# Kernel optimization log

Measured on AMD Instinct MI355X. Metric: run time of the kernel, lower is better.

Reference implementation:

```python
import jax, jax.numpy as jnp
import numpy as np

BS, TS, NE, ED = 32, 64, 64, 96
E = 256        # attn_embed_dim
H = 4          # attn_n_heads
HD = E // H    # head dim
RNN_H = 256
N_ACT = 32
NA = 16        # n_agents


def setup_inputs():
    key = jax.random.key(0)
    ks = jax.random.split(key, 40)
    entities = jax.random.normal(ks[0], (BS, TS, NE, ED), jnp.float32)
    obs_mask = jax.random.randint(ks[1], (BS, TS, NE, NE), 0, 2).astype(jnp.float32)  # 1 = masked
    entity_mask = (jax.random.uniform(ks[2], (BS, TS, NE)) < 0.1).astype(jnp.float32)  # 1 = inactive
    hidden_state = jnp.zeros((BS * NA, RNN_H), jnp.float32)
    it = iter(range(3, 40))
    def lin(fi, fo):
        return jax.random.normal(ks[next(it)], (fi, fo), jnp.float32) / np.sqrt(fi).astype(np.float32)
    p = dict(
        fc1_w=lin(ED, E), fc1_b=jnp.zeros((E,), jnp.float32),
        attn_in_w=lin(E, 3 * E), attn_out_w=lin(E, E), attn_out_b=jnp.zeros((E,), jnp.float32),
        fc2_w=lin(2 * E, RNN_H), fc2_b=jnp.zeros((RNN_H,), jnp.float32),
        gru_w_ih=lin(RNN_H, 3 * RNN_H), gru_w_hh=lin(RNN_H, 3 * RNN_H),
        gru_b_ih=jnp.zeros((3 * RNN_H,), jnp.float32), gru_b_hh=jnp.zeros((3 * RNN_H,), jnp.float32),
        fc3_w=lin(RNN_H, N_ACT), fc3_b=jnp.zeros((N_ACT,), jnp.float32),
        fcmsg1_w=lin(ED, E), fcmsg1_b=jnp.zeros((E,), jnp.float32),
        lmsg_in_w=lin(E, 3 * E), lmsg_out_w=lin(E, E), lmsg_out_b=jnp.zeros((E,), jnp.float32),
        gmsg_in_w=lin(E, 3 * E), gmsg_out_w=lin(E, E), gmsg_out_b=jnp.zeros((E,), jnp.float32),
        gate_in_w=lin(E, 3 * E), gate_out_w=lin(E, E), gate_out_b=jnp.zeros((E,), jnp.float32),
        gatefc1_w=lin(ED, E), gatefc1_b=jnp.zeros((E,), jnp.float32),
        gatefc2_w=lin(E, 2), gatefc2_b=jnp.zeros((2,), jnp.float32),
    )
    return dict(entities=entities, obs_mask=obs_mask, entity_mask=entity_mask,
                hidden_state=hidden_state, **p)


def _attn(x, in_w, out_w, out_b, pre_mask, post_mask):
    """REFIL EntityAttentionLayer: n_queries = NA agent rows, masks use 1 = masked."""
    B, ne, e = x.shape
    q, k, v = jnp.split(x @ in_w, 3, axis=-1)                       # each [B, ne, E]
    q = q[:, :NA].reshape(B, NA, H, HD).transpose(0, 2, 1, 3)        # [B, H, NA, HD]
    k = k.reshape(B, ne, H, HD).transpose(0, 2, 1, 3)                # [B, H, ne, HD]
    v = v.reshape(B, ne, H, HD).transpose(0, 2, 1, 3)
    logits = jnp.einsum('bhqd,bhkd->bhqk', q, k) / jnp.asarray(np.sqrt(HD), x.dtype)
    m = pre_mask[:, None, :NA, :]                                    # [B, 1, NA, ne]
    logits = jnp.where(m > 0, jnp.asarray(-1e9, x.dtype), logits)
    # softmax; zeroing masked cols also reproduces torch's NaN->0 for fully-masked rows
    w = jax.nn.softmax(logits, axis=-1) * (1.0 - m)
    out = jnp.einsum('bhqk,bhkd->bhqd', w, v).transpose(0, 2, 1, 3).reshape(B, NA, e)
    out = out @ out_w + out_b
    return out * (1.0 - post_mask[..., None])                        # masked_fill(post_mask, 0)


def _forward(entities, obs_mask, entity_mask, hidden_state,
             fc1_w, fc1_b, attn_in_w, attn_out_w, attn_out_b, fc2_w, fc2_b,
             gru_w_ih, gru_w_hh, gru_b_ih, gru_b_hh, fc3_w, fc3_b,
             fcmsg1_w, fcmsg1_b, lmsg_in_w, lmsg_out_w, lmsg_out_b,
             gmsg_in_w, gmsg_out_w, gmsg_out_b, gate_in_w, gate_out_w, gate_out_b,
             gatefc1_w, gatefc1_b, gatefc2_w, gatefc2_b):
    bs, ts, ne, ed = entities.shape
    B = bs * ts
    ent = entities.reshape(B, ne, ed)
    om = obs_mask.reshape(B, ne, ne)
    em = entity_mask.reshape(B, ne)
    agent_mask = em[:, :NA]                                          # [B, NA]
    full_obs_mask = 1.0 - (1.0 - agent_mask[:, None, :]) * (1.0 - agent_mask[:, :, None])

    x1 = jax.nn.relu(ent @ fc1_w + fc1_b)
    x2 = _attn(x1, attn_in_w, attn_out_w, attn_out_b, om, agent_mask)          # [B, NA, E]

    x1_msg = jax.nn.relu(ent @ fcmsg1_w + fcmsg1_b)
    x1_gate = jax.nn.relu(ent @ gatefc1_w + gatefc1_b)
    x2_msg = _attn(x1_msg, lmsg_in_w, lmsg_out_w, lmsg_out_b, om, agent_mask)  # [B, NA, E]
    x2_gate = _attn(x1_gate, gate_in_w, gate_out_w, gate_out_b, om, agent_mask)
    x2_gate = x2_gate @ gatefc2_w + gatefc2_b                                   # [B, NA, 2]

    # argmax of softmax == argmax of logits; gate in {0,1}, non-differentiable
    gate = jnp.argmax(x2_gate, axis=-1).astype(entities.dtype)
    gated_msg = x2_msg * gate[..., None]
    global_msg = _attn(gated_msg, gmsg_in_w, gmsg_out_w, gmsg_out_b,
                       full_obs_mask, agent_mask)                               # [B, NA, E]

    x3 = jax.nn.relu(jnp.concatenate([x2, global_msg], axis=-1) @ fc2_w + fc2_b)
    x3 = x3.reshape(bs, ts, NA, RNN_H)

    # GRU recurrence over ts via scan; hidden flattened to [bs*NA, RNN_H]
    h0 = hidden_state.reshape(-1, RNN_H)
    xs = x3.transpose(1, 0, 2, 3).reshape(ts, bs * NA, RNN_H)

    def step(h, x):
        gi = x @ gru_w_ih + gru_b_ih
        gh = h @ gru_w_hh + gru_b_hh
        ir, iz, inn = jnp.split(gi, 3, axis=-1)
        hr, hz, hn = jnp.split(gh, 3, axis=-1)
        r = jax.nn.sigmoid(ir + hr)
        z = jax.nn.sigmoid(iz + hz)
        n = jnp.tanh(inn + r * hn)
        h_new = (1.0 - z) * n + z * h
        return h_new, h_new

    _, hs = jax.lax.scan(step, h0, xs)                               # [ts, bs*NA, RNN_H]
    hs = hs.reshape(ts, bs, NA, RNN_H).transpose(1, 0, 2, 3)         # [bs, ts, NA, RNN_H]

    q = hs @ fc3_w + fc3_b                                           # [bs, ts, NA, N_ACT]
    am = agent_mask.reshape(bs, ts, NA, 1)
    q = q * (1.0 - am)                                               # masked_fill(agent_mask, 0)
    return q, hs, x2_gate


def reference(entities, obs_mask, entity_mask, hidden_state,
              fc1_w, fc1_b, attn_in_w, attn_out_w, attn_out_b, fc2_w, fc2_b,
              gru_w_ih, gru_w_hh, gru_b_ih, gru_b_hh, fc3_w, fc3_b,
              fcmsg1_w, fcmsg1_b, lmsg_in_w, lmsg_out_w, lmsg_out_b,
              gmsg_in_w, gmsg_out_w, gmsg_out_b, gate_in_w, gate_out_w, gate_out_b,
              gatefc1_w, gatefc1_b, gatefc2_w, gatefc2_b):
    return _forward(entities, obs_mask, entity_mask, hidden_state,
                    fc1_w, fc1_b, attn_in_w, attn_out_w, attn_out_b, fc2_w, fc2_b,
                    gru_w_ih, gru_w_hh, gru_b_ih, gru_b_hh, fc3_w, fc3_b,
                    fcmsg1_w, fcmsg1_b, lmsg_in_w, lmsg_out_w, lmsg_out_b,
                    gmsg_in_w, gmsg_out_w, gmsg_out_b, gate_in_w, gate_out_w, gate_out_b,
                    gatefc1_w, gatefc1_b, gatefc2_w, gatefc2_b)
```

## Files before the change

### kernel.cpp

```cpp
#include <hip/hip_runtime.h>


#define DEV __device__ __forceinline__

typedef _Float16 f16x8 __attribute__((ext_vector_type(8)));
typedef _Float16 f16x4 __attribute__((ext_vector_type(4)));
typedef float    f32x4 __attribute__((ext_vector_type(4)));
typedef float    f32x16 __attribute__((ext_vector_type(16)));

DEV f32x4 mfma16(f16x8 a, f16x8 b, f32x4 c){
  return __builtin_amdgcn_mfma_f32_16x16x32_f16(a, b, c, 0, 0, 0);
}
DEV f32x16 mfma32(f16x8 a, f16x8 b, f32x16 c){
  return __builtin_amdgcn_mfma_f32_32x32x16_f16(a, b, c, 0, 0, 0);
}

template<int MODE> struct AB {
  f16x8 hi, lo;
  DEV void mf(const AB& b, f32x4& c) const {
    if constexpr (MODE){
      c = mfma16(lo, b.hi, c);
      c = mfma16(hi, b.lo, c);
    }
    c = mfma16(hi, b.hi, c);
  }
};

template<int MODE> DEV AB<MODE> ldW(const _Float16* p, int losz){
  AB<MODE> r; r.hi = *(const f16x8*)p;
  if constexpr (MODE) r.lo = *(const f16x8*)(p + losz);
  return r;
}
template<int MODE> DEV AB<MODE> ldL(const _Float16* ph, const _Float16* pl){
  AB<MODE> r; r.hi = *(const f16x8*)ph;
  if constexpr (MODE) r.lo = *(const f16x8*)pl;
  return r;
}
template<int MODE> DEV AB<MODE> ldF(const float* p){
  AB<MODE> r;
  f32x4 v0 = *(const f32x4*)p, v1 = *(const f32x4*)(p + 4);
#pragma unroll
  for (int i = 0; i < 4; ++i){
    float a = v0[i], b = v1[i];
    _Float16 ah = (_Float16)a, bh = (_Float16)b;
    r.hi[i] = ah; r.hi[i+4] = bh;
    if constexpr (MODE){
      r.lo[i]   = (_Float16)(a - (float)ah);
      r.lo[i+4] = (_Float16)(b - (float)bh);
    }
  }
  return r;
}
template<int MODE> DEV void stL(_Float16* ph, _Float16* pl, int idx, float v){
  _Float16 h = (_Float16)v;
  ph[idx] = h;
  if constexpr (MODE) pl[idx] = (_Float16)(v - (float)h);
}

struct WJobs {
  const float* src[15];
  unsigned off[15];
  int K[15], N[15], mode[15];
};

__global__ __launch_bounds__(256) void k0_conv(WJobs jb, char* ws){
  const int job = blockIdx.y;
  const int K = jb.K[job], N = jb.N[job];
  const int total = K * N;
  _Float16* dh = (_Float16*)(ws + jb.off[job]);
  const float* src = jb.src[job];
  const int m = jb.mode[job];
  for (int idx = blockIdx.x*256 + threadIdx.x; idx < total; idx += gridDim.x*256){
    int n = idx / K, k = idx - n*K;
    float v = src[(size_t)k*N + n];
    _Float16 h = (_Float16)v;
    dh[idx] = h;
    if (m) dh[total + idx] = (_Float16)(v - (float)h);
  }
}

__global__ __launch_bounds__(256) void k0w_gate(
    const float* __restrict__ Wout, const float* __restrict__ Wg2,
    const float* __restrict__ bo,   const float* __restrict__ Win,
    _Float16* __restrict__ wveff, float* __restrict__ beff)
{
  __shared__ float weff_s[256*2];
  const int tid = threadIdx.x;
  {
    float a0 = 0.f, a1 = 0.f;
    const float* wr = Wout + (size_t)tid*256;
    for (int f = 0; f < 256; ++f){ float x = wr[f]; a0 += x*Wg2[2*f]; a1 += x*Wg2[2*f+1]; }
    weff_s[tid*2] = a0; weff_s[tid*2+1] = a1;
  }
  if (tid < 2){
    float s = 0.f;
    for (int f = 0; f < 256; ++f) s += bo[f]*Wg2[2*f + tid];
    beff[tid] = s;
  }
  __syncthreads();
  {
    const int j = tid;
    for (int n = 0; n < 16; ++n){
      float v = 0.f;
      if (n < 8){
        int h = n >> 1, c = n & 1;
        const float* wr = Win + (size_t)j*768 + 512 + h*64;
        const float* we = weff_s + (h*64)*2 + c;
        for (int d = 0; d < 64; ++d) v += wr[d]*we[2*d];
      }
      _Float16 hi = (_Float16)v;
      wveff[n*256 + j] = hi;
      wveff[16*256 + n*256 + j] = (_Float16)(v - (float)hi);
    }
  }
}

__global__ __launch_bounds__(512) void k1_all(
    const float* __restrict__ ent, const float* __restrict__ om, const float* __restrict__ em,
    const _Float16* __restrict__ W1a, const float* __restrict__ b1a,
    const _Float16* __restrict__ WINa,
    const _Float16* __restrict__ WOUTa, const float* __restrict__ boa,
    float* __restrict__ x2outa,
    const _Float16* __restrict__ W1b, const float* __restrict__ b1b,
    const _Float16* __restrict__ WINb,
    const _Float16* __restrict__ WOUTb, const float* __restrict__ bob,
    float* __restrict__ x2outb,
    const _Float16* __restrict__ W1g, const float* __restrict__ b1g,
    const _Float16* __restrict__ WINg,
    const _Float16* __restrict__ WVEFF,
    const float* __restrict__ beff, const float* __restrict__ gb2,
    float* __restrict__ og, float* __restrict__ gate)
{
  const int tid = threadIdx.x;
  const int w = tid >> 6, lg = (tid >> 4) & 3, li = tid & 15;
  extern __shared__ char smem[];

  if (blockIdx.x < 2048){
    const int br = blockIdx.x >> 10;
    const int p  = blockIdx.x & 1023;
    const int bb2[2] = { 2*p, 2*p + 1 };
    const _Float16* W1   = br ? W1b   : W1a;
    const float*    b1   = br ? b1b   : b1a;
    const _Float16* WIN  = br ? WINb  : WINa;
    const _Float16* WOUT = br ? WOUTb : WOUTa;
    const float*    bo   = br ? bob   : boa;
    float*          x2out= br ? x2outb: x2outa;

    const int wi = w & 3, ih = w >> 2;
    const int l = tid & 63;
    const int r32 = l & 31, kh = (l >> 5)*8;

    _Float16* x1   = (_Float16*)smem;
    _Float16* Ks   = (_Float16*)(smem + 67584);
    _Float16* Vs   = (_Float16*)(smem + 86016);
    _Float16* Qful = (_Float16*)(smem + 104448);
    float*    lgs  = (float*)(smem + 121344);
    _Float16* Ps   = (_Float16*)(smem + 130560);
    _Float16* outp = (_Float16*)(smem + 135168);

    {
      const int b = bb2[ih];
      _Float16* x1p = x1 + ih*16896;
      const int mt = wi & 1, ntb = (wi >> 1)*4;
      f32x16 acc0 = 0.f, acc1 = 0.f, acc2 = 0.f, acc3 = 0.f;
#pragma unroll
      for (int kk = 0; kk < 6; ++kk){
        AB<0> a = ldF<0>(ent + ((size_t)b*64 + mt*32 + r32)*96 + kk*16 + kh);
        f16x8 B0 = *(const f16x8*)(W1 + (size_t)((ntb + 0)*32 + r32)*96 + kk*16 + kh);
        f16x8 B1 = *(const f16x8*)(W1 + (size_t)((ntb + 1)*32 + r32)*96 + kk*16 + kh);
        f16x8 B2 = *(const f16x8*)(W1 + (size_t)((ntb + 2)*32 + r32)*96 + kk*16 + kh);
        f16x8 B3 = *(const f16x8*)(W1 + (size_t)((ntb + 3)*32 + r32)*96 + kk*16 + kh);
        acc0 = mfma32(a.hi, B0, acc0);
        acc1 = mfma32(a.hi, B1, acc1);
        acc2 = mfma32(a.hi, B2, acc2);
        acc3 = mfma32(a.hi, B3, acc3);
      }
#pragma unroll
      for (int s = 0; s < 4; ++s){
        const f32x16& ac = (s == 0) ? acc0 : (s == 1) ? acc1 : (s == 2) ? acc2 : acc3;
        int col = (ntb + s)*32 + r32;
        float bias = b1[col];
#pragma unroll
        for (int reg = 0; reg < 16; ++reg){
          int row = (reg & 3) + 8*(reg >> 2) + 4*(l >> 5);
          x1p[(mt*32 + row)*264 + col] = (_Float16)fmaxf(ac[reg] + bias, 0.f);
        }
      }
    }
    __syncthreads();

    {
      f32x16 acc = 0.f;
      const int itq = r32 >> 4, qr = r32 & 15;
      for (int kk = 0; kk < 16; ++kk){
        f16x8 A = *(const f16x8*)(x1 + itq*16896 + qr*264 + kk*16 + kh);
        f16x8 B = *(const f16x8*)(WIN + (size_t)(w*32 + r32)*256 + kk*16 + kh);
        acc = mfma32(A, B, acc);
      }
#pragma unroll
      for (int reg = 0; reg < 16; ++reg){
        int row = (reg & 3) + 8*(reg >> 2) + 4*(l >> 5);
        Qful[(row >> 4)*4224 + (row & 15)*264 + w*32 + r32] = (_Float16)acc[reg];
      }
    }
    __syncthreads();

    for (int h = 0; h < 4; ++h){
      if (w < 4){
        const int kt = w >> 1, dt = w & 1;
        f32x16 acc0 = 0.f, acc1 = 0.f;
        for (int kk = 0; kk < 16; ++kk){
          int ao = (kt*32 + r32)*264 + kk*16 + kh;
          f16x8 A0 = *(const f16x8*)(x1 + ao);
          f16x8 A1 = *(const f16x8*)(x1 + 16896 + ao);
          f16x8 B = *(const f16x8*)(WIN + (size_t)(256 + 64*h + dt*32 + r32)*256 + kk*16 + kh);
          acc0 = mfma32(A0, B, acc0);
          acc1 = mfma32(A1, B, acc1);
        }
#pragma unroll
        for (int reg = 0; reg < 16; ++reg){
          int row = (reg & 3) + 8*(reg >> 2) + 4*(l >> 5);
          Ks[(kt*32 + row)*72 + dt*32 + r32]        = (_Float16)acc0[reg];
          Ks[4608 + (kt*32 + row)*72 + dt*32 + r32] = (_Float16)acc1[reg];
        }
      } else {
        const int wv = w - 4;
        const int kt = wv >> 1, dt = wv & 1;
        f32x16 acc0 = 0.f, acc1 = 0.f;
        for (int kk = 0; kk < 16; ++kk){
          int ao = (kt*32 + r32)*264 + kk*16 + kh;
          f16x8 A0 = *(const f16x8*)(x1 + ao);
          f16x8 A1 = *(const f16x8*)(x1 + 16896 + ao);
          f16x8 B = *(const f16x8*)(WIN + (size_t)(512 + 64*h + dt*32 + r32)*256 + kk*16 + kh);
          acc0 = mfma32(A0, B, acc0);
          acc1 = mfma32(A1, B, acc1);
        }
#pragma unroll
        for (int rr = 0; rr < 4; ++rr){
          f16x4 p0, p1;
#pragma unroll
          for (int q4 = 0; q4 < 4; ++q4){
            p0[q4] = (_Float16)acc0[rr*4 + q4];
            p1[q4] = (_Float16)acc1[rr*4 + q4];
          }
          int key = kt*32 + rr*8 + 4*(l >> 5);
          *(f16x4*)(Vs + (dt*32 + r32)*72 + key)        = p0;
          *(f16x4*)(Vs + 4608 + (dt*32 + r32)*72 + key) = p1;
        }
      }
      __syncthreads();
      {
        const int b = bb2[ih];
        f32x4 acc = 0.f;
#pragma unroll
        for (int kk = 0; kk < 2; ++kk){
          f16x8 A = *(const f16x8*)(Qful + ih*4224 + li*264 + 64*h + kk*32 + lg*8);
          f16x8 B = *(const f16x8*)(Ks + ih*4608 + (16*wi + li)*72 + kk*32 + lg*8);
          acc = mfma16(A, B, acc);
        }
#pragma unroll
        for (int j = 0; j < 4; ++j){
          int q = 4*lg + j, key = 16*wi + li;
          float v = acc[j] * 0.125f;
          float m = om[((size_t)b*64 + q)*64 + key];
          if (m > 0.f) v = -1e9f;
          lgs[ih*1152 + q*72 + key] = v;
        }
      }
      __syncthreads();
      {
        const int it = tid >> 8, q = (tid >> 4) & 15, i16 = tid & 15;
        const int b = bb2[it];
        float pv[4], mx = -3e38f;
#pragma unroll
        for (int u = 0; u < 4; ++u){ pv[u] = lgs[it*1152 + q*72 + i16 + 16*u]; mx = fmaxf(mx, pv[u]); }
#pragma unroll
        for (int d = 1; d < 16; d <<= 1) mx = fmaxf(mx, __shfl_xor(mx, d, 16));
        float s = 0.f;
#pragma unroll
        for (int u = 0; u < 4; ++u){ pv[u] = expf(pv[u] - mx); s += pv[u]; }
#pragma unroll
        for (int d = 1; d < 16; d <<= 1) s += __shfl_xor(s, d, 16);
#pragma unroll
        for (int u = 0; u < 4; ++u){
          int key = i16 + 16*u;
          float m = om[((size_t)b*64 + q)*64 + key];
          Ps[it*1152 + q*72 + key] = (_Float16)((pv[u]/s)*(1.f - m));
        }
      }
      __syncthreads();
      {
        f32x4 acc = 0.f;
#pragma unroll
        for (int kk = 0; kk < 2; ++kk){
          f16x8 A = *(const f16x8*)(Ps + ih*1152 + li*72 + kk*32 + lg*8);
          f16x8 B = *(const f16x8*)(Vs + ih*4608 + (16*wi + li)*72 + kk*32 + lg*8);
          acc = mfma16(A, B, acc);
        }
#pragma unroll
        for (int j = 0; j < 4; ++j)
          outp[ih*4224 + (4*lg + j)*264 + 64*h + 16*wi + li] = (_Float16)acc[j];
      }
      __syncthreads();
    }

    {
      f32x16 acc = 0.f;
      const int ito = r32 >> 4, qr = r32 & 15;
      for (int kk = 0; kk < 16; ++kk){
        f16x8 A = *(const f16x8*)(outp + ito*4224 + qr*264 + kk*16 + kh);
        f16x8 B = *(const f16x8*)(WOUT + (size_t)(w*32 + r32)*256 + kk*16 + kh);
        acc = mfma32(A, B, acc);
      }
      int col = w*32 + r32;
      float bias = bo[col];
#pragma unroll
      for (int reg = 0; reg < 16; ++reg){
        int row = (reg & 3) + 8*(reg >> 2) + 4*(l >> 5);
        int it2 = row >> 4, q2 = row & 15;
        const int b = bb2[it2];
        float v = (acc[reg] + bias) * (1.f - em[(size_t)b*64 + q2]);
        x2out[((size_t)b*16 + q2)*256 + col] = v;
      }
    }
    return;
  }

  {
    constexpr int W1SZ = 96*256, WINSZ = 256*768, WVSZ = 16*256;
    const int b = blockIdx.x - 2048;
    const int l = tid & 63;
    const int r32 = l & 31, kh = (l >> 5)*8;

    char* sp = smem;
    _Float16* x1h = (_Float16*)sp; sp += 64*264*2;
    _Float16* x1l = (_Float16*)sp; sp += 64*264*2;
    _Float16* Kh  = (_Float16*)sp; sp += 64*72*2;
    _Float16* Kl  = (_Float16*)sp; sp += 64*72*2;
    _Float16* Qh  = (_Float16*)sp; sp += 16*264*2;
    _Float16* Ql  = (_Float16*)sp; sp += 16*264*2;
    float*    lgs = (float*)sp;    sp += 16*72*4;
    float*    Ps  = (float*)sp;    sp += 16*66*4;
    float*    v2s = (float*)sp;    sp += 64*18*4;
    float*  ogacc = (float*)sp;    sp += 32*4;
    float*  Kpart = (float*)sp;    sp += 8192*4;

    {
      const int mt = w & 1, ntb = (w >> 1)*2;
      f32x16 acc0 = 0.f, acc1 = 0.f;
#pragma unroll
      for (int kk = 0; kk < 6; ++kk){
        AB<1> a = ldF<1>(ent + ((size_t)b*64 + mt*32 + r32)*96 + kk*16 + kh);
#pragma unroll
        for (int s = 0; s < 2; ++s){
          const _Float16* bp = W1g + (size_t)((ntb + s)*32 + r32)*96 + kk*16 + kh;
          f16x8 Bh = *(const f16x8*)bp;
          f16x8 Bl = *(const f16x8*)(bp + W1SZ);
          f32x16& ac = s ? acc1 : acc0;
          ac = mfma32(a.lo, Bh, ac);
          ac = mfma32(a.hi, Bl, ac);
          ac = mfma32(a.hi, Bh, ac);
        }
      }
#pragma unroll
      for (int s = 0; s < 2; ++s){
        const f32x16& ac = s ? acc1 : acc0;
        int col = (ntb + s)*32 + r32;
        float bias = b1g[col];
#pragma unroll
        for (int reg = 0; reg < 16; ++reg){
          int row = (reg & 3) + 8*(reg >> 2) + 4*(l >> 5);
          stL<1>(x1h, x1l, (mt*32 + row)*264 + col, fmaxf(ac[reg] + bias, 0.f));
        }
      }
    }
    if (tid < 32) ogacc[tid] = 0.f;
    __syncthreads();

    {
#pragma unroll
      for (int s = 0; s < 2; ++s){
        int nt = w + s*8;
        f32x4 acc = 0.f;
        for (int kk = 0; kk < 8; ++kk){
          int ao = li*264 + kk*32 + lg*8;
          AB<1> a = ldL<1>(x1h + ao, x1l + ao);
          AB<1> bb = ldW<1>(WINg + (size_t)(nt*16 + li)*256 + kk*32 + lg*8, WINSZ);
          a.mf(bb, acc);
        }
#pragma unroll
        for (int j = 0; j < 4; ++j)
          stL<1>(Qh, Ql, (4*lg + j)*264 + nt*16 + li, acc[j]);
      }
      if (w < 4){
        f32x4 acc = 0.f;
        for (int kk = 0; kk < 8; ++kk){
          int ao = (w*16 + li)*264 + kk*32 + lg*8;
          AB<1> a = ldL<1>(x1h + ao, x1l + ao);
          AB<1> bb = ldW<1>(WVEFF + (size_t)li*256 + kk*32 + lg*8, WVSZ);
          a.mf(bb, acc);
        }
#pragma unroll
        for (int j = 0; j < 4; ++j)
          v2s[(w*16 + 4*lg + j)*18 + li] = acc[j];
      }
    }
    __syncthreads();

    for (int h = 0; h < 4; ++h){
      {
        const int t = w & 3, kt = t >> 1, dt = t & 1, khalf = w >> 2;
        f32x16 acc = 0.f;
#pragma unroll
        for (int k8 = 0; k8 < 8; ++k8){
          int ko = (khalf*8 + k8)*16 + kh;
          int ao = (kt*32 + r32)*264 + ko;
          f16x8 ah = *(const f16x8*)(x1h + ao);
          f16x8 al = *(const f16x8*)(x1l + ao);
          const _Float16* bp = WINg + (size_t)(256 + h*64 + dt*32 + r32)*256 + ko;
          f16x8 Bh = *(const f16x8*)bp;
          f16x8 Bl = *(const f16x8*)(bp + WINSZ);
          acc = mfma32(al, Bh, acc);
          acc = mfma32(ah, Bl, acc);
          acc = mfma32(ah, Bh, acc);
        }
#pragma unroll
        for (int reg = 0; reg < 16; ++reg){
          int row = (reg & 3) + 8*(reg >> 2) + 4*(l >> 5);
          Kpart[((khalf*4 + t)*32 + row)*32 + r32] = acc[reg];
        }
      }
      __syncthreads();
      {
        for (int e = tid; e < 4096; e += 512){
          float s2 = Kpart[e] + Kpart[4096 + e];
          int t2 = e >> 10, idx = e & 1023, row = idx >> 5, col = idx & 31;
          stL<1>(Kh, Kl, ((t2 >> 1)*32 + row)*72 + (t2 & 1)*32 + col, s2);
        }
      }
      __syncthreads();
      if (w < 4){
        f32x4 acc = 0.f;
#pragma unroll
        for (int kk = 0; kk < 2; ++kk){
          int ao = li*264 + h*64 + kk*32 + lg*8;
          AB<1> a = ldL<1>(Qh + ao, Ql + ao);
          int bo_ = (16*w + li)*72 + kk*32 + lg*8;
          AB<1> bb = ldL<1>(Kh + bo_, Kl + bo_);
          a.mf(bb, acc);
        }
#pragma unroll
        for (int j = 0; j < 4; ++j){
          int q = 4*lg + j, key = 16*w + li;
          float v = acc[j] * 0.125f;
          float m = om[((size_t)b*64 + q)*64 + key];
          if (m > 0.f) v = -1e9f;
          lgs[q*72 + key] = v;
        }
      }
      __syncthreads();
      if (tid < 256){
        int q = tid >> 4, i16 = tid & 15;
        float pv[4], mx = -3e38f;
#pragma unroll
        for (int u = 0; u < 4; ++u){ pv[u] = lgs[q*72 + i16 + 16*u]; mx = fmaxf(mx, pv[u]); }
#pragma unroll
        for (int d = 1; d < 16; d <<= 1) mx = fmaxf(mx, __shfl_xor(mx, d, 16));
        float s = 0.f;
#pragma unroll
        for (int u = 0; u < 4; ++u){ pv[u] = expf(pv[u] - mx); s += pv[u]; }
#pragma unroll
        for (int d = 1; d < 16; d <<= 1) s += __shfl_xor(s, d, 16);
#pragma unroll
        for (int u = 0; u < 4; ++u){
          int key = i16 + 16*u;
          float m = om[((size_t)b*64 + q)*64 + key];
          Ps[q*66 + key] = (pv[u]/s)*(1.f - m);
        }
      }
      __syncthreads();
      if (tid < 256){
        int q = tid >> 4, l16 = tid & 15;
        float a0 = 0.f, a1 = 0.f;
#pragma unroll
        for (int u = 0; u < 4; ++u){
          int k = l16 + 16*u;
          float p2 = Ps[q*66 + k];
          a0 += p2 * v2s[k*18 + h*2];
          a1 += p2 * v2s[k*18 + h*2 + 1];
        }
#pragma unroll
        for (int d = 1; d < 16; d <<= 1){ a0 += __shfl_xor(a0, d, 16); a1 += __shfl_xor(a1, d, 16); }
        if (l16 == 0){ ogacc[q*2] += a0; ogacc[q*2 + 1] += a1; }
      }
      __syncthreads();
    }
    if (tid < 16){
      int q = tid;
      float am = em[(size_t)b*64 + q];
      float g0 = (1.f - am)*(ogacc[2*q]     + beff[0]) + gb2[0];
      float g1 = (1.f - am)*(ogacc[2*q + 1] + beff[1]) + gb2[1];
      og[((size_t)b*16 + q)*2]     = g0;
      og[((size_t)b*16 + q)*2 + 1] = g1;
      gate[(size_t)b*16 + q] = (g1 > g0) ? 1.f : 0.f;
    }
  }
}

__global__ __launch_bounds__(256) void k2_global(
    const float* __restrict__ em,
    const float* __restrict__ x2, const float* __restrict__ x2m,
    const float* __restrict__ gate,
    const _Float16* __restrict__ GMIN, const _Float16* __restrict__ GMOUT, const float* __restrict__ gob,
    const _Float16* __restrict__ FC2T, const float* __restrict__ fc2b,
    const _Float16* __restrict__ GIHT, const float* __restrict__ gib,
    float* __restrict__ gi)
{
  const int p = blockIdx.x;
  const int tid = threadIdx.x;
  const int w = tid >> 6, lg = (tid >> 4) & 3, li = tid & 15;
  const int l = tid & 63;
  const int r32 = l & 31, kh = (l >> 5)*8;

  extern __shared__ char smem[];
  float*    gate_s = (float*)smem;
  _Float16* gm_s   = (_Float16*)(smem + 128);
  _Float16* Q2     = (_Float16*)(smem + 17024);
  _Float16* K2s    = (_Float16*)(smem + 21632);
  _Float16* Vt2    = (_Float16*)(smem + 26240);
  float*    lg2    = (float*)(smem + 36480);
  _Float16* P2     = (_Float16*)(smem + 39552);
  _Float16* outp   = (_Float16*)(smem + 42112);
  _Float16* cat_s  = (_Float16*)(smem + 59008);
  _Float16* x3_s   = (_Float16*)(smem + 92288);

  if (tid < 32){
    int it = tid >> 4, q = tid & 15;
    gate_s[it*16 + q] = gate[(size_t)(2*p + it)*16 + q];
  }
  __syncthreads();
#pragma unroll
  for (int it = 0; it < 2; ++it){
    const int b = 2*p + it;
    for (int idx = tid; idx < 4096; idx += 256){
      int q = idx >> 8, d = idx & 255;
      gm_s[it*4224 + q*264 + d]  = (_Float16)(x2m[((size_t)b*16 + q)*256 + d] * gate_s[it*16 + q]);
      cat_s[it*8320 + q*520 + d] = (_Float16)(x2[((size_t)b*16 + q)*256 + d]);
    }
  }
  for (int idx = tid; idx < 2*64*40; idx += 256) Vt2[idx] = (_Float16)0.f;
  for (int idx = tid; idx < 2*16*40; idx += 256) P2[idx] = (_Float16)0.f;
  __syncthreads();
  for (int h = 0; h < 4; ++h){
    {
      f32x4 aq0 = 0.f, aq1 = 0.f, ak0 = 0.f, ak1 = 0.f, av0 = 0.f, av1 = 0.f;
      for (int kk = 0; kk < 8; ++kk){
        f16x8 A0 = *(const f16x8*)(gm_s + li*264 + kk*32 + lg*8);
        f16x8 A1 = *(const f16x8*)(gm_s + 4224 + li*264 + kk*32 + lg*8);
        f16x8 Bq = *(const f16x8*)(GMIN + (size_t)(      64*h + 16*w + li)*256 + kk*32 + lg*8);
        f16x8 Bk = *(const f16x8*)(GMIN + (size_t)(256 + 64*h + 16*w + li)*256 + kk*32 + lg*8);
        f16x8 Bv = *(const f16x8*)(GMIN + (size_t)(512 + 64*h + 16*w + li)*256 + kk*32 + lg*8);
        aq0 = mfma16(A0, Bq, aq0); aq1 = mfma16(A1, Bq, aq1);
        ak0 = mfma16(A0, Bk, ak0); ak1 = mfma16(A1, Bk, ak1);
        av0 = mfma16(A0, Bv, av0); av1 = mfma16(A1, Bv, av1);
      }
#pragma unroll
      for (int j = 0; j < 4; ++j){
        int rw = 4*lg + j, dim = 16*w + li;
        Q2[rw*72 + dim]         = (_Float16)aq0[j];
        Q2[1152 + rw*72 + dim]  = (_Float16)aq1[j];
        K2s[rw*72 + dim]        = (_Float16)ak0[j];
        K2s[1152 + rw*72 + dim] = (_Float16)ak1[j];
        Vt2[dim*40 + rw]        = (_Float16)av0[j];
        Vt2[2560 + dim*40 + rw] = (_Float16)av1[j];
      }
    }
    __syncthreads();
    if (w < 2){
      const int it = w, b = 2*p + it;
      f32x4 acc = 0.f;
#pragma unroll
      for (int kk = 0; kk < 2; ++kk){
        f16x8 A = *(const f16x8*)(Q2  + it*1152 + li*72 + kk*32 + lg*8);
        f16x8 B = *(const f16x8*)(K2s + it*1152 + li*72 + kk*32 + lg*8);
        acc = mfma16(A, B, acc);
      }
      float amk = em[(size_t)b*64 + li];
#pragma unroll
      for (int j = 0; j < 4; ++j){
        int q = 4*lg + j;
        float amq = em[(size_t)b*64 + q];
        float m = 1.f - (1.f - amq)*(1.f - amk);
        float v = acc[j]*0.125f;
        if (m > 0.f) v = -1e9f;
        lg2[it*384 + q*24 + li] = v;
      }
    }
    __syncthreads();
    {
      int q = tid >> 4, key = tid & 15;
#pragma unroll
      for (int it = 0; it < 2; ++it){
        const int b = 2*p + it;
        float v = lg2[it*384 + q*24 + key];
        float mx = v;
#pragma unroll
        for (int d = 1; d < 16; d <<= 1) mx = fmaxf(mx, __shfl_xor(mx, d, 16));
        float pe = expf(v - mx);
        float s = pe;
#pragma unroll
        for (int d = 1; d < 16; d <<= 1) s += __shfl_xor(s, d, 16);
        float amq = em[(size_t)b*64 + q], amk = em[(size_t)b*64 + key];
        float m = 1.f - (1.f - amq)*(1.f - amk);
        P2[it*640 + q*40 + key] = (_Float16)((pe/s)*(1.f - m));
      }
    }
    __syncthreads();
    {
#pragma unroll
      for (int it = 0; it < 2; ++it){
        f32x4 acc = 0.f;
        f16x8 A = *(const f16x8*)(P2 + it*640 + li*40 + lg*8);
        f16x8 B = *(const f16x8*)(Vt2 + it*2560 + (16*w + li)*40 + lg*8);
        acc = mfma16(A, B, acc);
#pragma unroll
        for (int j = 0; j < 4; ++j)
          outp[it*4224 + (4*lg + j)*264 + 64*h + 16*w + li] = (_Float16)acc[j];
      }
    }
    __syncthreads();
  }
  {
    const int ito = r32 >> 4, qr = r32 & 15;
#pragma unroll
    for (int s = 0; s < 2; ++s){
      int nt = 2*w + s;
      f32x16 acc = 0.f;
      for (int kk = 0; kk < 16; ++kk){
        f16x8 A = *(const f16x8*)(outp + ito*4224 + qr*264 + kk*16 + kh);
        f16x8 B = *(const f16x8*)(GMOUT + (size_t)(nt*32 + r32)*256 + kk*16 + kh);
        acc = mfma32(A, B, acc);
      }
      int col = nt*32 + r32;
      float bias = gob[col];
#pragma unroll
      for (int reg = 0; reg < 16; ++reg){
        int row = (reg & 3) + 8*(reg >> 2) + 4*(l >> 5);
        int it2 = row >> 4, q2 = row & 15;
        float m = 1.f - em[(size_t)(2*p + it2)*64 + q2];
        cat_s[it2*8320 + q2*520 + 256 + col] = (_Float16)((acc[reg] + bias)*m);
      }
    }
  }
  __syncthreads();
  {
    const int ito = r32 >> 4, qr = r32 & 15;
#pragma unroll
    for (int s = 0; s < 2; ++s){
      int nt = 2*w + s;
      f32x16 acc = 0.f;
      for (int kk = 0; kk < 32; ++kk){
        f16x8 A = *(const f16x8*)(cat_s + ito*8320 + qr*520 + kk*16 + kh);
        f16x8 B = *(const f16x8*)(FC2T + (size_t)(nt*32 + r32)*512 + kk*16 + kh);
        acc = mfma32(A, B, acc);
      }
      int col = nt*32 + r32;
      float bias = fc2b[col];
#pragma unroll
      for (int reg = 0; reg < 16; ++reg){
        int row = (reg & 3) + 8*(reg >> 2) + 4*(l >> 5);
        int it2 = row >> 4, q2 = row & 15;
        x3_s[it2*4224 + q2*264 + col] = (_Float16)fmaxf(acc[reg] + bias, 0.f);
      }
    }
  }
  __syncthreads();
  {
    const int r0 = ((2*p) >> 6)*16, t0 = (2*p) & 63;
    const int ito = r32 >> 4, qr = r32 & 15;
#pragma unroll
    for (int s = 0; s < 6; ++s){
      int nt = 6*w + s;
      f32x16 acc = 0.f;
      for (int kk = 0; kk < 16; ++kk){
        f16x8 A = *(const f16x8*)(x3_s + ito*4224 + qr*264 + kk*16 + kh);
        f16x8 B = *(const f16x8*)(GIHT + (size_t)(nt*32 + r32)*256 + kk*16 + kh);
        acc = mfma32(A, B, acc);
      }
      int col = nt*32 + r32;
      float bias = gib[col];
#pragma unroll
      for (int reg = 0; reg < 16; ++reg){
        int row = (reg & 3) + 8*(reg >> 2) + 4*(l >> 5);
        int it2 = row >> 4, q2 = row & 15;
        gi[((size_t)((r0 + q2)*64 + t0 + it2))*768 + col] = acc[reg] + bias;
      }
    }
  }
}

__global__ __launch_bounds__(512) void k3_gru(
    const _Float16* __restrict__ WHH, const float* __restrict__ bhh,
    const float* __restrict__ gi, const float* __restrict__ h0,
    float* __restrict__ hs)
{
  const int rb = blockIdx.x;
  const int row0 = rb * 16;
  const int tid = threadIdx.x;
  const int w = tid >> 6, lg = (tid >> 4) & 3, li = tid & 15;

  extern __shared__ char smem3[];
  _Float16* hf16 = (_Float16*)smem3;
  float* hf32 = (float*)(smem3 + 8448);
  float* gh   = (float*)(smem3 + 8448 + 16640);
  float* bhs  = (float*)(smem3 + 8448 + 16640 + 49664);

  for (int idx = tid; idx < 768; idx += 512) bhs[idx] = bhh[idx];
  for (int idx = tid; idx < 4096; idx += 512){
    int r = idx >> 8, d = idx & 255;
    float v = h0[(size_t)(row0 + r)*256 + d];
    hf32[r*260 + d] = v;
    hf16[r*264 + d] = (_Float16)v;
  }
  __syncthreads();

  const int er = tid >> 5;
  const int dd = (tid & 31) * 8;

  for (int t = 0; t < 64; ++t){
    const float* gp = gi + ((size_t)(row0 + er)*64 + t)*768 + dd;
    f32x4 gr[2], gz[2], gn[2];
#pragma unroll
    for (int v = 0; v < 2; ++v){
      gr[v] = *(const f32x4*)(gp + v*4);
      gz[v] = *(const f32x4*)(gp + 256 + v*4);
      gn[v] = *(const f32x4*)(gp + 512 + v*4);
    }
    f16x8 a[8];
#pragma unroll
    for (int kk = 0; kk < 8; ++kk)
      a[kk] = *(const f16x8*)(hf16 + li*264 + kk*32 + lg*8);
    f32x4 acc[6];
#pragma unroll
    for (int c = 0; c < 6; ++c) acc[c] = 0.f;
#pragma unroll
    for (int c = 0; c < 6; ++c){
      const _Float16* bp = WHH + (size_t)(w*96 + c*16 + li)*256 + lg*8;
#pragma unroll
      for (int kk = 0; kk < 8; ++kk)
        acc[c] = mfma16(a[kk], *(const f16x8*)(bp + kk*32), acc[c]);
    }
#pragma unroll
    for (int c = 0; c < 6; ++c){
      int col = w*96 + c*16 + li;
#pragma unroll
      for (int j = 0; j < 4; ++j)
        gh[(4*lg + j)*776 + col] = acc[c][j];
    }
    __syncthreads();
    {
      float* hp32 = hf32 + er*260 + dd;
      float* hsp  = hs + ((size_t)(rb*64 + t)*16 + er)*256 + dd;
      f16x8 hv8;
#pragma unroll
      for (int v = 0; v < 2; ++v){
        f32x4 xr = *(const f32x4*)(gh + er*776 +       dd + v*4);
        f32x4 xz = *(const f32x4*)(gh + er*776 + 256 + dd + v*4);
        f32x4 xn = *(const f32x4*)(gh + er*776 + 512 + dd + v*4);
        f32x4 hold = *(const f32x4*)(hp32 + v*4);
        f32x4 hout;
#pragma unroll
        for (int e = 0; e < 4; ++e){
          int d = dd + v*4 + e;
          float rr_ = 1.f/(1.f + __expf(-(gr[v][e] + xr[e] + bhs[d])));
          float zz  = 1.f/(1.f + __expf(-(gz[v][e] + xz[e] + bhs[256 + d])));
          float pre = gn[v][e] + rr_*(xn[e] + bhs[512 + d]);
          float nn  = 1.f - 2.f/(1.f + __expf(2.f*pre));
          float hv = (1.f - zz)*nn + zz*hold[e];
          hout[e] = hv;
          hv8[v*4 + e] = (_Float16)hv;
        }
        *(f32x4*)(hp32 + v*4) = hout;
        *(f32x4*)(hsp + v*4)  = hout;
      }
      *(f16x8*)(hf16 + er*264 + dd) = hv8;
    }
    __syncthreads();
  }
}

__global__ __launch_bounds__(256) void k4_q(
    const _Float16* __restrict__ FC3T, const float* __restrict__ fc3b,
    const float* __restrict__ em, const float* __restrict__ hs, float* __restrict__ qo)
{
  const int tid = threadIdx.x;
  const int w = tid >> 6, lg = (tid >> 4) & 3, li = tid & 15;
  const int rb = blockIdx.x*64 + 16*w;
  f32x4 acc[2];
#pragma unroll
  for (int c = 0; c < 2; ++c) acc[c] = 0.f;
  for (int kk = 0; kk < 8; ++kk){
    const float* ap = hs + (size_t)(rb + li)*256 + kk*32 + lg*8;
    f32x4 v0 = *(const f32x4*)ap, v1 = *(const f32x4*)(ap + 4);
    f16x8 A;
#pragma unroll
    for (int e = 0; e < 4; ++e){ A[e] = (_Float16)v0[e]; A[e+4] = (_Float16)v1[e]; }
#pragma unroll
    for (int c = 0; c < 2; ++c){
      f16x8 B = *(const f16x8*)(FC3T + (size_t)(16*c + li)*256 + kk*32 + lg*8);
      acc[c] = mfma16(A, B, acc[c]);
    }
  }
#pragma unroll
  for (int c = 0; c < 2; ++c){
    int col = 16*c + li;
    float bias = fc3b[col];
#pragma unroll
    for (int j = 0; j < 4; ++j){
      int row = rb + 4*lg + j;
      float am = em[(size_t)(row >> 4)*64 + (row & 15)];
      qo[(size_t)row*32 + col] = (acc[c][j] + bias)*(1.f - am);
    }
  }
}

extern "C" void kernel_launch(void* const* d_in, const int* in_sizes, int n_in,
                              void* d_out, int out_size, void* d_ws, size_t ws_size,
                              hipStream_t stream)
{
  constexpr size_t OFF_FC1T   = 0;
  constexpr size_t OFF_MSG1T  = 49152;
  constexpr size_t OFF_AINT   = 98304;
  constexpr size_t OFF_LINT   = 491520;
  constexpr size_t OFF_AOUTT  = 884736;
  constexpr size_t OFF_LOUTT  = 1015808;
  constexpr size_t OFF_GMINT  = 1146880;
  constexpr size_t OFF_GMOUTT = 1540096;
  constexpr size_t OFF_FC2T   = 1671168;
  constexpr size_t OFF_GIHT   = 1933312;
  constexpr size_t OFF_GHHT   = 2326528;
  constexpr size_t OFF_FC3T   = 2719744;
  constexpr size_t OFF_G1T    = 2736128;
  constexpr size_t OFF_GINT   = 2834432;
  constexpr size_t OFF_WVEFF  = 3620864;
  constexpr size_t OFF_BEFF   = 3637248;
  constexpr size_t OFF_GATE   = 3637504;
  constexpr size_t OFF_X2     = 3768576;
  constexpr size_t OFF_X2M    = 37323008;
  constexpr size_t OFF_GI     = 70877440;
  constexpr size_t NEED       = 171540736;
  if (ws_size < NEED) return;

  char* ws = (char*)d_ws;
  const float* ent = (const float*)d_in[0];
  const float* om  = (const float*)d_in[1];
  const float* em  = (const float*)d_in[2];

  WJobs jb{};
  int nj = 0;
  auto addj = [&](int src_idx, size_t off, int K, int N, int m){
    jb.src[nj] = (const float*)d_in[src_idx]; jb.off[nj] = (unsigned)off;
    jb.K[nj] = K; jb.N[nj] = N; jb.mode[nj] = m; ++nj;
  };
  addj(4,  OFF_FC1T,   96, 256, 0);
  addj(17, OFF_MSG1T,  96, 256, 0);
  addj(6,  OFF_AINT,  256, 768, 0);
  addj(19, OFF_LINT,  256, 768, 0);
  addj(7,  OFF_AOUTT, 256, 256, 0);
  addj(20, OFF_LOUTT, 256, 256, 0);
  addj(22, OFF_GMINT, 256, 768, 0);
  addj(23, OFF_GMOUTT,256, 256, 0);
  addj(9,  OFF_FC2T,  512, 256, 0);
  addj(11, OFF_GIHT,  256, 768, 0);
  addj(12, OFF_GHHT,  256, 768, 0);
  addj(15, OFF_FC3T,  256,  32, 0);
  addj(28, OFF_G1T,    96, 256, 1);
  addj(25, OFF_GINT,  256, 768, 1);
  k0_conv<<<dim3(96, nj), 256, 0, stream>>>(jb, ws);

  k0w_gate<<<1, 256, 0, stream>>>(
      (const float*)d_in[26], (const float*)d_in[30],
      (const float*)d_in[27], (const float*)d_in[25],
      (_Float16*)(ws + OFF_WVEFF), (float*)(ws + OFF_BEFF));

  constexpr int SMB = 156672, SMK2 = 109184, SM3 = 77824;
  (void)hipFuncSetAttribute(reinterpret_cast<const void*>(&k1_all),
                            hipFuncAttributeMaxDynamicSharedMemorySize, SMB);
  (void)hipFuncSetAttribute(reinterpret_cast<const void*>(&k2_global),
                            hipFuncAttributeMaxDynamicSharedMemorySize, SMK2);
  (void)hipFuncSetAttribute(reinterpret_cast<const void*>(&k3_gru),
                            hipFuncAttributeMaxDynamicSharedMemorySize, SM3);

  float* qout = (float*)d_out;
  float* hsout = qout + 1048576;
  float* gout = qout + 9437184;

  k1_all<<<4096, 512, SMB, stream>>>(ent, om, em,
      (const _Float16*)(ws + OFF_FC1T),  (const float*)d_in[5],
      (const _Float16*)(ws + OFF_AINT),
      (const _Float16*)(ws + OFF_AOUTT), (const float*)d_in[8],
      (float*)(ws + OFF_X2),
      (const _Float16*)(ws + OFF_MSG1T), (const float*)d_in[18],
      (const _Float16*)(ws + OFF_LINT),
      (const _Float16*)(ws + OFF_LOUTT), (const float*)d_in[21],
      (float*)(ws + OFF_X2M),
      (const _Float16*)(ws + OFF_G1T),   (const float*)d_in[29],
      (const _Float16*)(ws + OFF_GINT),
      (const _Float16*)(ws + OFF_WVEFF),
      (const float*)(ws + OFF_BEFF), (const float*)d_in[31],
      gout, (float*)(ws + OFF_GATE));

  k2_global<<<1024, 256, SMK2, stream>>>(em,
      (const float*)(ws + OFF_X2), (const float*)(ws + OFF_X2M),
      (const float*)(ws + OFF_GATE),
      (const _Float16*)(ws + OFF_GMINT), (const _Float16*)(ws + OFF_GMOUTT), (const float*)d_in[24],
      (const _Float16*)(ws + OFF_FC2T), (const float*)d_in[10],
      (const _Float16*)(ws + OFF_GIHT), (const float*)d_in[13],
      (float*)(ws + OFF_GI));

  k3_gru<<<32, 512, SM3, stream>>>(
      (const _Float16*)(ws + OFF_GHHT), (const float*)d_in[14],
      (const float*)(ws + OFF_GI), (const float*)d_in[3], hsout);

  k4_q<<<512, 256, 0, stream>>>(
      (const _Float16*)(ws + OFF_FC3T), (const float*)d_in[16],
      em, hsout, qout);
}
```

Before: 1.154 ms.

## Hoist global-message QKV projection out of per-head loop into one 32x32 MFMA GEMM

In k2_global, the per-head Q/K/V projection with 16x16 MFMAs and a barrier per head is replaced by a single upfront projection of all heads using 32x32x16 MFMAs. Results go to full-width Qall/Kall/Vtall shared buffers, and the per-head attention reads slices from them. Shared memory is re-laid out and grows to 131200 bytes, with cat_s aliasing Qall and the x2 copy into cat_s deferred until after attention. This removes one barrier per head and gives the projection better MFMA shapes, but the larger LDS footprint may reduce occupancy.

```diff
diff --git a/kernel.cpp b/kernel.cpp
--- a/kernel.cpp
+++ b/kernel.cpp
@@ -525,14 +525,14 @@
   extern __shared__ char smem[];
   float*    gate_s = (float*)smem;
   _Float16* gm_s   = (_Float16*)(smem + 128);
-  _Float16* Q2     = (_Float16*)(smem + 17024);
-  _Float16* K2s    = (_Float16*)(smem + 21632);
-  _Float16* Vt2    = (_Float16*)(smem + 26240);
-  float*    lg2    = (float*)(smem + 36480);
-  _Float16* P2     = (_Float16*)(smem + 39552);
-  _Float16* outp   = (_Float16*)(smem + 42112);
-  _Float16* cat_s  = (_Float16*)(smem + 59008);
-  _Float16* x3_s   = (_Float16*)(smem + 92288);
+  float*    lg2    = (float*)(smem + 17024);
+  _Float16* P2     = (_Float16*)(smem + 20096);
+  _Float16* outp   = (_Float16*)(smem + 22656);
+  _Float16* x3_s   = (_Float16*)(smem + 39552);
+  _Float16* Vtall  = (_Float16*)(smem + 56448);
+  _Float16* Qall   = (_Float16*)(smem + 97408);
+  _Float16* Kall   = (_Float16*)(smem + 114304);
+  _Float16* cat_s  = (_Float16*)(smem + 97408);
 
   if (tid < 32){
     int it = tid >> 4, q = tid & 15;
@@ -544,45 +544,47 @@
     const int b = 2*p + it;
     for (int idx = tid; idx < 4096; idx += 256){
       int q = idx >> 8, d = idx & 255;
-      gm_s[it*4224 + q*264 + d]  = (_Float16)(x2m[((size_t)b*16 + q)*256 + d] * gate_s[it*16 + q]);
-      cat_s[it*8320 + q*520 + d] = (_Float16)(x2[((size_t)b*16 + q)*256 + d]);
-    }
-  }
-  for (int idx = tid; idx < 2*64*40; idx += 256) Vt2[idx] = (_Float16)0.f;
+      gm_s[it*4224 + q*264 + d] = (_Float16)(x2m[((size_t)b*16 + q)*256 + d] * gate_s[it*16 + q]);
+    }
+  }
+  for (int idx = tid; idx < 10240; idx += 256) ((unsigned*)Vtall)[idx] = 0u;
   for (int idx = tid; idx < 2*16*40; idx += 256) P2[idx] = (_Float16)0.f;
   __syncthreads();
+
+  {
+    const int itq = r32 >> 4, qr = r32 & 15;
+#pragma unroll
+    for (int s = 0; s < 6; ++s){
+      int nt = 6*w + s;
+      f32x16 acc = 0.f;
+      for (int kk = 0; kk < 16; ++kk){
+        f16x8 A = *(const f16x8*)(gm_s + itq*4224 + qr*264 + kk*16 + kh);
+        f16x8 B = *(const f16x8*)(GMIN + (size_t)(nt*32 + r32)*256 + kk*16 + kh);
+        acc = mfma32(A, B, acc);
+      }
+      int sec = nt >> 3;
+      int hcol = (nt & 7)*32 + r32;
+#pragma unroll
+      for (int reg = 0; reg < 16; ++reg){
+        int row = (reg & 3) + 8*(reg >> 2) + 4*(l >> 5);
+        int it2 = row >> 4, q2 = row & 15;
+        _Float16 v = (_Float16)acc[reg];
+        if (sec == 0)      Qall[it2*4224 + q2*264 + hcol] = v;
+        else if (sec == 1) Kall[it2*4224 + q2*264 + hcol] = v;
+        else               Vtall[it2*10240 + hcol*40 + q2] = v;
+      }
+    }
+  }
+  __syncthreads();
+
   for (int h = 0; h < 4; ++h){
-    {
-      f32x4 aq0 = 0.f, aq1 = 0.f, ak0 = 0.f, ak1 = 0.f, av0 = 0.f, av1 = 0.f;
-      for (int kk = 0; kk < 8; ++kk){
-        f16x8 A0 = *(const f16x8*)(gm_s + li*264 + kk*32 + lg*8);
-        f16x8 A1 = *(const f16x8*)(gm_s + 4224 + li*264 + kk*32 + lg*8);
-        f16x8 Bq = *(const f16x8*)(GMIN + (size_t)(      64*h + 16*w + li)*256 + kk*32 + lg*8);
-        f16x8 Bk = *(const f16x8*)(GMIN + (size_t)(256 + 64*h + 16*w + li)*256 + kk*32 + lg*8);
-        f16x8 Bv = *(const f16x8*)(GMIN + (size_t)(512 + 64*h + 16*w + li)*256 + kk*32 + lg*8);
-        aq0 = mfma16(A0, Bq, aq0); aq1 = mfma16(A1, Bq, aq1);
-        ak0 = mfma16(A0, Bk, ak0); ak1 = mfma16(A1, Bk, ak1);
-        av0 = mfma16(A0, Bv, av0); av1 = mfma16(A1, Bv, av1);
-      }
-#pragma unroll
-      for (int j = 0; j < 4; ++j){
-        int rw = 4*lg + j, dim = 16*w + li;
-        Q2[rw*72 + dim]         = (_Float16)aq0[j];
-        Q2[1152 + rw*72 + dim]  = (_Float16)aq1[j];
-        K2s[rw*72 + dim]        = (_Float16)ak0[j];
-        K2s[1152 + rw*72 + dim] = (_Float16)ak1[j];
-        Vt2[dim*40 + rw]        = (_Float16)av0[j];
-        Vt2[2560 + dim*40 + rw] = (_Float16)av1[j];
-      }
-    }
-    __syncthreads();
     if (w < 2){
       const int it = w, b = 2*p + it;
       f32x4 acc = 0.f;
 #pragma unroll
       for (int kk = 0; kk < 2; ++kk){
-        f16x8 A = *(const f16x8*)(Q2  + it*1152 + li*72 + kk*32 + lg*8);
-        f16x8 B = *(const f16x8*)(K2s + it*1152 + li*72 + kk*32 + lg*8);
+        f16x8 A = *(const f16x8*)(Qall + it*4224 + li*264 + 64*h + kk*32 + lg*8);
+        f16x8 B = *(const f16x8*)(Kall + it*4224 + li*264 + 64*h + kk*32 + lg*8);
         acc = mfma16(A, B, acc);
       }
       float amk = em[(size_t)b*64 + li];
@@ -621,7 +623,7 @@
       for (int it = 0; it < 2; ++it){
         f32x4 acc = 0.f;
         f16x8 A = *(const f16x8*)(P2 + it*640 + li*40 + lg*8);
-        f16x8 B = *(const f16x8*)(Vt2 + it*2560 + (16*w + li)*40 + lg*8);
+        f16x8 B = *(const f16x8*)(Vtall + it*10240 + (size_t)(64*h + 16*w + li)*40 + lg*8);
         acc = mfma16(A, B, acc);
 #pragma unroll
         for (int j = 0; j < 4; ++j)
@@ -649,6 +651,14 @@
         int it2 = row >> 4, q2 = row & 15;
         float m = 1.f - em[(size_t)(2*p + it2)*64 + q2];
         cat_s[it2*8320 + q2*520 + 256 + col] = (_Float16)((acc[reg] + bias)*m);
+      }
+    }
+#pragma unroll
+    for (int it = 0; it < 2; ++it){
+      const int b = 2*p + it;
+      for (int idx = tid; idx < 4096; idx += 256){
+        int q = idx >> 8, d = idx & 255;
+        cat_s[it*8320 + q*520 + d] = (_Float16)(x2[((size_t)b*16 + q)*256 + d]);
       }
     }
   }
@@ -883,7 +893,7 @@
       (const float*)d_in[27], (const float*)d_in[25],
       (_Float16*)(ws + OFF_WVEFF), (float*)(ws + OFF_BEFF));
 
-  constexpr int SMB = 156672, SMK2 = 109184, SM3 = 77824;
+  constexpr int SMB = 156672, SMK2 = 131200, SM3 = 77824;
   (void)hipFuncSetAttribute(reinterpret_cast<const void*>(&k1_all),
                             hipFuncAttributeMaxDynamicSharedMemorySize, SMB);
   (void)hipFuncSetAttribute(reinterpret_cast<const void*>(&k2_global),
```

Result: no change. 1.144 ms (-0.9%).
